# Performance work log

Hardware: AMD Instinct MI355X
Metric: run time of the kernel (lower is better)

## Reference

```python
import jax, jax.numpy as jnp
import numpy as np

N = 50000          # nodes (B-rep faces)
E = 1600000        # edges (face adjacency, avg degree 32)
GRID = 8           # UV sample grid
HEADS = 4
DH = 32            # per-head dim (heads*DH = 128)
NUM_CLASSES = 25


def _conv(x, w, b):
    # x: [N,C,H,W], w: [O,I,3,3], SAME padding, stride 1
    y = jax.lax.conv_general_dilated(x, w, (1, 1), 'SAME',
                                     dimension_numbers=('NCHW', 'OIHW', 'NCHW'))
    return y + b[None, :, None, None]


def gated_gat(x, edge_index, edge_attr, W, b, We, be, a_src, a_dst, a_edge, Wg, bg):
    # Multi-head GAT with edge-feature attention term and sigmoid edge gate.
    n = x.shape[0]
    h = (x @ W + b).reshape(n, HEADS, DH)                 # [N,H,D]
    src, dst = edge_index[0], edge_index[1]
    h_src = h[src]                                        # [E,H,D] gather
    h_dst = h[dst]                                        # [E,H,D] gather
    e_feat = (edge_attr @ We + be).reshape(-1, HEADS, DH) # [E,H,D]
    logits = jax.nn.leaky_relu(
        (h_src * a_src).sum(-1) + (h_dst * a_dst).sum(-1) + (e_feat * a_edge).sum(-1),
        negative_slope=0.2)                               # [E,H]
    # segment softmax over incoming edges of each dst node
    m = jax.ops.segment_max(logits, dst, num_segments=n)  # [N,H]
    ex = jnp.exp(logits - m[dst])
    denom = jax.ops.segment_sum(ex, dst, num_segments=n)
    alpha = ex / (denom[dst] + 1e-16)                     # [E,H]
    gate = jax.nn.sigmoid(edge_attr @ Wg + bg)            # [E,1] scalar edge gate
    msg = (h_src + e_feat) * alpha[..., None] * gate[:, :, None]  # [E,H,D]
    out = jax.ops.segment_sum(msg, dst, num_segments=n)   # [N,H,D] scatter-add
    return jax.nn.elu(out.reshape(n, HEADS * DH))


def setup_inputs() -> dict:
    key = jax.random.key(0)
    ks = jax.random.split(key, 32)
    def nrm(k, shape, s=0.05):
        return jax.random.normal(k, shape, jnp.float32) * s
    z = lambda *s: jnp.zeros(s, jnp.float32)
    return dict(
        x_vis=jax.random.normal(ks[0], (N, 6, GRID, GRID), jnp.float32),
        x_sym=jax.random.normal(ks[1], (N, 3), jnp.float32),
        edge_index=jax.random.randint(ks[2], (2, E), 0, N),
        edge_attr=jax.random.uniform(ks[3], (E, 2), jnp.float32),
        # UVEncoder: conv(6->32) -> conv(32->64) -> global avg pool -> fc(64->128)
        conv1_w=nrm(ks[4], (32, 6, 3, 3)), conv1_b=z(32),
        conv2_w=nrm(ks[5], (64, 32, 3, 3)), conv2_b=z(64),
        uvfc_w=nrm(ks[6], (64, 128)), uvfc_b=z(128),
        # SymbolicEncoder: fc(3->64) -> relu -> fc(64->64) -> relu
        sym1_w=nrm(ks[7], (3, 64)), sym1_b=z(64),
        sym2_w=nrm(ks[8], (64, 64)), sym2_b=z(64),
        # GatedGAT layer 1 (192 -> 128, heads=4, edge_dim=2)
        g1_W=nrm(ks[9], (192, 128)), g1_b=z(128),
        g1_We=nrm(ks[10], (2, 128)), g1_be=z(128),
        g1_asrc=nrm(ks[11], (HEADS, DH)), g1_adst=nrm(ks[12], (HEADS, DH)),
        g1_aedge=nrm(ks[13], (HEADS, DH)),
        g1_Wg=nrm(ks[14], (2, 1)), g1_bg=z(1),
        # GatedGAT layer 2 (128 -> 128)
        g2_W=nrm(ks[15], (128, 128)), g2_b=z(128),
        g2_We=nrm(ks[16], (2, 128)), g2_be=z(128),
        g2_asrc=nrm(ks[17], (HEADS, DH)), g2_adst=nrm(ks[18], (HEADS, DH)),
        g2_aedge=nrm(ks[19], (HEADS, DH)),
        g2_Wg=nrm(ks[20], (2, 1)), g2_bg=z(1),
        # classifier: fc(128->64) -> relu -> (dropout eval noop) -> fc(64->25)
        cls1_w=nrm(ks[21], (128, 64)), cls1_b=z(64),
        cls2_w=nrm(ks[22], (64, NUM_CLASSES)), cls2_b=z(NUM_CLASSES),
    )


def reference(x_vis, x_sym, edge_index, edge_attr,
              conv1_w, conv1_b, conv2_w, conv2_b, uvfc_w, uvfc_b,
              sym1_w, sym1_b, sym2_w, sym2_b,
              g1_W, g1_b, g1_We, g1_be, g1_asrc, g1_adst, g1_aedge, g1_Wg, g1_bg,
              g2_W, g2_b, g2_We, g2_be, g2_asrc, g2_adst, g2_aedge, g2_Wg, g2_bg,
              cls1_w, cls1_b, cls2_w, cls2_b):
    # UVEncoder
    h = jax.nn.relu(_conv(x_vis, conv1_w, conv1_b))
    h = jax.nn.relu(_conv(h, conv2_w, conv2_b))
    v_vis = h.mean(axis=(2, 3)) @ uvfc_w + uvfc_b          # [N,128]
    # SymbolicEncoder
    v_sym = jax.nn.relu(x_sym @ sym1_w + sym1_b)
    v_sym = jax.nn.relu(v_sym @ sym2_w + sym2_b)           # [N,64]
    x = jnp.concatenate([v_vis, v_sym], axis=1)            # [N,192]
    x = gated_gat(x, edge_index, edge_attr, g1_W, g1_b, g1_We, g1_be,
                  g1_asrc, g1_adst, g1_aedge, g1_Wg, g1_bg)
    x = gated_gat(x, edge_index, edge_attr, g2_W, g2_b, g2_We, g2_be,
                  g2_asrc, g2_adst, g2_aedge, g2_Wg, g2_bg)
    h = jax.nn.relu(x @ cls1_w + cls1_b)
    return h @ cls2_w + cls2_b                             # [N,25]
```

## Files before the change

kernel.cpp:

```cpp
#include <hip/hip_runtime.h>

#define NND 50000
#define NE  1600000
#define CAP 72

typedef __attribute__((ext_vector_type(8))) short bf16x8;
typedef __attribute__((ext_vector_type(4))) float f32x4;

__device__ __forceinline__ float leaky02(float x){ return x > 0.f ? x : 0.2f*x; }
__device__ __forceinline__ unsigned short f2bf(float f){
  unsigned u = __float_as_uint(f);
  u = (u + 0x7fffu + ((u >> 16) & 1u)) >> 16;
  return (unsigned short)u;
}
__device__ __forceinline__ float bf2f(unsigned short h){
  return __uint_as_float(((unsigned)h) << 16);
}
__device__ __forceinline__ unsigned cvt_pk_bf16(float lo, float hi){
  unsigned r;
  asm("v_cvt_pk_bf16_f32 %0, %1, %2" : "=v"(r) : "v"(lo), "v"(hi));
  return r;
}
__device__ __forceinline__ bf16x8 ld_frag(const unsigned short* p){
  return __builtin_bit_cast(bf16x8, *(const uint4*)p);
}

__global__ __launch_bounds__(256) void prep_mega(
    const float* __restrict__ w1, const float* __restrict__ w2,
    unsigned short* __restrict__ W1t, unsigned short* __restrict__ W2t,
    const float* __restrict__ fcw, const float* __restrict__ fcb,
    const float* __restrict__ g1W, const float* __restrict__ g1b,
    float* __restrict__ Weff, float* __restrict__ beff,
    const float* __restrict__ g2W,
    unsigned short* __restrict__ G1h, unsigned short* __restrict__ G1l,
    unsigned short* __restrict__ G2h, unsigned short* __restrict__ G2l,
    int* __restrict__ cnt)
{
  int b = blockIdx.x, t = threadIdx.x;
  if (b == 0){
    for (int i = t; i < 3072; i += 256){
      int j = i & 7, oc = (i >> 3) & 31, g = (i >> 8) & 3, m = i >> 10;
      int tap = m*4 + g;
      float v = (tap < 9 && j < 6) ? w1[oc*54 + j*9 + tap] : 0.f;
      W1t[i] = f2bf(v);
    }
  } else if (b == 1){
    for (int i = t; i < 18432; i += 256){
      int j = i & 7, oc = (i >> 3) & 63, g = (i >> 9) & 3, tap = i >> 11;
      int ic = g*8 + j;
      W2t[i] = f2bf(w2[oc*288 + ic*9 + tap]);
    }
  } else if (b < 66){
    int idx = (b - 2)*256 + t;
    int r = idx >> 7, c = idx & 127;
    float acc;
    if (r < 64){
      acc = 0.f;
      #pragma unroll 4
      for (int m = 0; m < 128; m++) acc += fcw[r*128 + m] * g1W[m*128 + c];
    } else {
      acc = g1W[(64 + r)*128 + c];
    }
    Weff[idx] = acc;
    if (b == 2 && t < 128){
      float bacc = g1b[t];
      #pragma unroll 4
      for (int m = 0; m < 128; m++) bacc = fmaf(fcb[m], g1W[m*128 + t], bacc);
      beff[t] = bacc;
    }
  } else if (b < 194){
    int sub = b - 66;
    const float* W = (sub < 64) ? Weff : g2W;
    unsigned short* Wh = (sub < 64) ? G1h : G2h;
    unsigned short* Wl = (sub < 64) ? G1l : G2l;
    int i = (sub & 63)*256 + t;
    int j = i & 7, lx = (i >> 3) & 63, nt = (i >> 9) & 7, ks = i >> 12;
    int k = ks*32 + (lx >> 4)*8 + j;
    int col = nt*16 + (lx & 15);
    float v = W[k*128 + col];
    unsigned short h16 = f2bf(v);
    Wh[i] = h16;
    Wl[i] = f2bf(v - bf2f(h16));
  } else {
    int i = (b - 194)*256 + t;
    if (i < NND) cnt[i] = 0;
  }
}

__global__ __launch_bounds__(256) void scatter_kernel(const int* __restrict__ ei,
                                                      const float* __restrict__ ea,
                                                      int* __restrict__ cnt,
                                                      int2* __restrict__ srcattr){
  int e = blockIdx.x*256 + threadIdx.x;
  if (e < NE){
    int dstn = ei[NE + e];
    int pos  = atomicAdd(&cnt[dstn], 1);
    if (pos < CAP){
      float2 a = *(const float2*)(ea + 2*e);
      unsigned pa = (unsigned)f2bf(a.x) | ((unsigned)f2bf(a.y) << 16);
      srcattr[(unsigned)dstn*CAP + pos] = make_int2(ei[e], (int)pa);
    }
  }
}

__global__ __launch_bounds__(256, 2) void uv_mfma_kernel(
    const float* __restrict__ x_vis, const float* __restrict__ x_sym,
    const unsigned short* __restrict__ W1t, const unsigned short* __restrict__ W2t,
    const float* __restrict__ b1, const float* __restrict__ b2,
    const float* __restrict__ s1w, const float* __restrict__ s1b,
    const float* __restrict__ s2w, const float* __restrict__ s2b,
    float* __restrict__ x128)
{
  __shared__ __align__(16) unsigned short xic[4*800];
  __shared__ __align__(16) unsigned short c1p[4*4000];
  __shared__ float symh[4][64];

  const int t = threadIdx.x;
  const int w = t >> 6, l = t & 63;
  const int g = l >> 4, r16 = l & 15;
  const int xb = r16 & 7, yb = r16 >> 3;
  const int n = blockIdx.x*4 + w;

  uint4 z4 = {0,0,0,0};
  if (l < 36){
    int y, x;
    if (l < 10){ y = 0; x = l; }
    else if (l < 20){ y = 9; x = l - 10; }
    else if (l < 28){ y = l - 19; x = 0; }
    else { y = l - 27; x = 9; }
    *(uint4*)(xic + w*800 + (y*10 + x)*8) = z4;
    uint4* cp = (uint4*)(c1p + w*4000 + (y*10 + x)*40);
    cp[0] = z4; cp[1] = z4; cp[2] = z4; cp[3] = z4;
  }

  {
    const float* xv = x_vis + (size_t)n*384;
    int y = l >> 3, x = l & 7;
    float v0 = xv[l], v1 = xv[64+l], v2 = xv[128+l];
    float v3 = xv[192+l], v4 = xv[256+l], v5 = xv[320+l];
    uint4 pk;
    pk.x = cvt_pk_bf16(v0, v1);
    pk.y = cvt_pk_bf16(v2, v3);
    pk.z = cvt_pk_bf16(v4, v5);
    pk.w = 0u;
    *(uint4*)(xic + w*800 + ((y+1)*10 + (x+1))*8) = pk;
  }
  asm volatile("" ::: "memory");

  uint4 B1[3][2];
  #pragma unroll
  for (int m = 0; m < 3; m++)
    #pragma unroll
    for (int nt = 0; nt < 2; nt++)
      B1[m][nt] = *(const uint4*)(W1t + m*1024 + g*256 + (nt*16 + r16)*8);

  const int t0 = g;     const int dy0 = t0/3, dx0 = t0%3;
  const int t1 = 4 + g; const int dy1 = t1/3, dx1 = t1%3;
  const int dy2 = 2, dx2 = 2;

  const float b1a = b1[r16], b1c = b1[16 + r16];
  f32x4 acc1[4][2];
  #pragma unroll
  for (int mt = 0; mt < 4; mt++){
    acc1[mt][0] = (f32x4){b1a, b1a, b1a, b1a};
    acc1[mt][1] = (f32x4){b1c, b1c, b1c, b1c};
  }
  const unsigned short* xn = xic + w*800;
  #pragma unroll
  for (int mt = 0; mt < 4; mt++){
    const int Y = mt*2 + yb;
    bf16x8 A0 = ld_frag(xn + (Y+dy0)*80 + (xb+dx0)*8);
    bf16x8 A1 = ld_frag(xn + (Y+dy1)*80 + (xb+dx1)*8);
    bf16x8 A2 = ld_frag(xn + (Y+dy2)*80 + (xb+dx2)*8);
    #pragma unroll
    for (int nt = 0; nt < 2; nt++){
      acc1[mt][nt] = __builtin_amdgcn_mfma_f32_16x16x32_bf16(A0, __builtin_bit_cast(bf16x8, B1[0][nt]), acc1[mt][nt], 0,0,0);
      acc1[mt][nt] = __builtin_amdgcn_mfma_f32_16x16x32_bf16(A1, __builtin_bit_cast(bf16x8, B1[1][nt]), acc1[mt][nt], 0,0,0);
      acc1[mt][nt] = __builtin_amdgcn_mfma_f32_16x16x32_bf16(A2, __builtin_bit_cast(bf16x8, B1[2][nt]), acc1[mt][nt], 0,0,0);
    }
  }
  unsigned short* cn = c1p + w*4000;
  #pragma unroll
  for (int mt = 0; mt < 4; mt++)
    #pragma unroll
    for (int nt = 0; nt < 2; nt++)
      #pragma unroll
      for (int jp = 0; jp < 2; jp++){
        float v0 = acc1[mt][nt][2*jp];     v0 = v0 > 0.f ? v0 : 0.f;
        float v1 = acc1[mt][nt][2*jp + 1]; v1 = v1 > 0.f ? v1 : 0.f;
        unsigned pk = cvt_pk_bf16(v0, v1);
        int r0 = g*4 + 2*jp, r1 = r0 + 1;
        int y0 = mt*2 + (r0 >> 3), x0 = r0 & 7;
        int y1 = mt*2 + (r1 >> 3), x1 = r1 & 7;
        cn[((y0+1)*10 + (x0+1))*40 + nt*16 + r16] = (unsigned short)pk;
        cn[((y1+1)*10 + (x1+1))*40 + nt*16 + r16] = (unsigned short)(pk >> 16);
      }
  asm volatile("" ::: "memory");

  float pooled4[4];
  #pragma unroll
  for (int ph = 0; ph < 2; ph++){
    const int ntA = 2*ph, ntB = 2*ph + 1;
    const float bA = b2[ntA*16 + r16], bB = b2[ntB*16 + r16];
    f32x4 accA[4], accB[4];
    #pragma unroll
    for (int mt = 0; mt < 4; mt++){
      accA[mt] = (f32x4){bA, bA, bA, bA};
      accB[mt] = (f32x4){bB, bB, bB, bB};
    }
    #pragma unroll
    for (int tap = 0; tap < 9; tap++){
      const int dy = tap/3, dx = tap%3;
      uint4 BvA = *(const uint4*)(W2t + tap*2048 + g*512 + (ntA*16 + r16)*8);
      uint4 BvB = *(const uint4*)(W2t + tap*2048 + g*512 + (ntB*16 + r16)*8);
      uint4 Av[4];
      #pragma unroll
      for (int mt = 0; mt < 4; mt++){
        int Y = mt*2 + yb + dy, X = xb + dx;
        Av[mt] = *(const uint4*)(cn + (Y*10 + X)*40 + g*8);
      }
      #pragma unroll
      for (int mt = 0; mt < 4; mt++){
        accA[mt] = __builtin_amdgcn_mfma_f32_16x16x32_bf16(
            __builtin_bit_cast(bf16x8, Av[mt]), __builtin_bit_cast(bf16x8, BvA), accA[mt], 0,0,0);
        accB[mt] = __builtin_amdgcn_mfma_f32_16x16x32_bf16(
            __builtin_bit_cast(bf16x8, Av[mt]), __builtin_bit_cast(bf16x8, BvB), accB[mt], 0,0,0);
      }
    }
    float sA = 0.f, sB = 0.f;
    #pragma unroll
    for (int mt = 0; mt < 4; mt++)
      #pragma unroll
      for (int j = 0; j < 4; j++){
        float vA = accA[mt][j]; sA += (vA > 0.f ? vA : 0.f);
        float vB = accB[mt][j]; sB += (vB > 0.f ? vB : 0.f);
      }
    pooled4[ph*2]     = sA;
    pooled4[ph*2 + 1] = sB;
  }

  float* xo = x128 + (size_t)n*128;
  #pragma unroll
  for (int k = 0; k < 4; k++){
    pooled4[k] += __shfl_xor(pooled4[k], 16);
    pooled4[k] += __shfl_xor(pooled4[k], 32);
  }
  if (l < 16){
    #pragma unroll
    for (int k = 0; k < 4; k++)
      xo[k*16 + l] = pooled4[k] * (1.f/64.f);
  }
  {
    const float* xs = x_sym + (size_t)n*3;
    float a = s1b[l] + xs[0]*s1w[l] + xs[1]*s1w[64+l] + xs[2]*s1w[128+l];
    symh[w][l] = a > 0.f ? a : 0.f;
  }
  asm volatile("" ::: "memory");
  {
    float a = s2b[l];
    #pragma unroll 8
    for (int k = 0; k < 64; k++) a = fmaf(symh[w][k], s2w[k*64 + l], a);
    xo[64 + l] = a > 0.f ? a : 0.f;
  }
}

template<int K>
__global__ __launch_bounds__(256) void node_gemm(
    const float* __restrict__ xin,
    const unsigned short* __restrict__ Wh, const unsigned short* __restrict__ Wl,
    const float* __restrict__ b,
    const float* __restrict__ asrc, const float* __restrict__ adst,
    unsigned short* __restrict__ h_out, float* __restrict__ s_out, float* __restrict__ d_out)
{
  const int w = threadIdx.x >> 6, l = threadIdx.x & 63;
  const int g = l >> 4, r16 = l & 15;
  const int rowbase = blockIdx.x*16;
  const int nt0 = 2*w, nt1 = 2*w + 1;

  f32x4 acc0, acc1;
  {
    float b0 = b[nt0*16 + r16], b1v = b[nt1*16 + r16];
    acc0 = (f32x4){b0, b0, b0, b0};
    acc1 = (f32x4){b1v, b1v, b1v, b1v};
  }

  const float* xr = xin + (size_t)(rowbase + r16)*K + g*8;
  #pragma unroll
  for (int ks = 0; ks < K/32; ks++){
    float4 xa = *(const float4*)(xr + ks*32);
    float4 xb = *(const float4*)(xr + ks*32 + 4);
    float xs[8] = {xa.x,xa.y,xa.z,xa.w,xb.x,xb.y,xb.z,xb.w};
    uint4 hpk, lpk;
    unsigned* hp = (unsigned*)&hpk;
    unsigned* lp = (unsigned*)&lpk;
    #pragma unroll
    for (int p = 0; p < 4; p++){
      unsigned ph = cvt_pk_bf16(xs[2*p], xs[2*p+1]);
      float r0 = xs[2*p]   - __uint_as_float(ph << 16);
      float r1 = xs[2*p+1] - __uint_as_float(ph & 0xffff0000u);
      hp[p] = ph;
      lp[p] = cvt_pk_bf16(r0, r1);
    }
    bf16x8 Ah = __builtin_bit_cast(bf16x8, hpk);
    bf16x8 Al = __builtin_bit_cast(bf16x8, lpk);
    const int fo0 = (((ks*8 + nt0)*64 + l)*8);
    const int fo1 = (((ks*8 + nt1)*64 + l)*8);
    bf16x8 Bh0 = ld_frag(Wh + fo0), Bl0 = ld_frag(Wl + fo0);
    bf16x8 Bh1 = ld_frag(Wh + fo1), Bl1 = ld_frag(Wl + fo1);
    acc0 = __builtin_amdgcn_mfma_f32_16x16x32_bf16(Ah, Bh0, acc0, 0,0,0);
    acc0 = __builtin_amdgcn_mfma_f32_16x16x32_bf16(Al, Bh0, acc0, 0,0,0);
    acc0 = __builtin_amdgcn_mfma_f32_16x16x32_bf16(Ah, Bl0, acc0, 0,0,0);
    acc1 = __builtin_amdgcn_mfma_f32_16x16x32_bf16(Ah, Bh1, acc1, 0,0,0);
    acc1 = __builtin_amdgcn_mfma_f32_16x16x32_bf16(Al, Bh1, acc1, 0,0,0);
    acc1 = __builtin_amdgcn_mfma_f32_16x16x32_bf16(Ah, Bl1, acc1, 0,0,0);
  }

  #pragma unroll
  for (int jp = 0; jp < 2; jp++){
    unsigned p0 = cvt_pk_bf16(acc0[2*jp], acc0[2*jp+1]);
    unsigned p1 = cvt_pk_bf16(acc1[2*jp], acc1[2*jp+1]);
    size_t ra = (size_t)(rowbase + g*4 + 2*jp)*128;
    size_t rb = (size_t)(rowbase + g*4 + 2*jp + 1)*128;
    h_out[ra + nt0*16 + r16] = (unsigned short)p0;
    h_out[rb + nt0*16 + r16] = (unsigned short)(p0 >> 16);
    h_out[ra + nt1*16 + r16] = (unsigned short)p1;
    h_out[rb + nt1*16 + r16] = (unsigned short)(p1 >> 16);
  }

  float as0 = asrc[nt0*16 + r16], as1 = asrc[nt1*16 + r16];
  float ad0 = adst[nt0*16 + r16], ad1 = adst[nt1*16 + r16];
  float sp[4], dp[4];
  #pragma unroll
  for (int j = 0; j < 4; j++){
    sp[j] = acc0[j]*as0 + acc1[j]*as1;
    dp[j] = acc0[j]*ad0 + acc1[j]*ad1;
  }
  #pragma unroll
  for (int o = 1; o < 16; o <<= 1)
    #pragma unroll
    for (int j = 0; j < 4; j++){
      sp[j] += __shfl_xor(sp[j], o);
      dp[j] += __shfl_xor(dp[j], o);
    }
  if (r16 == 0)
    #pragma unroll
    for (int j = 0; j < 4; j++)
      s_out[(rowbase + g*4 + j)*4 + w] = sp[j];
  if (r16 == 1)
    #pragma unroll
    for (int j = 0; j < 4; j++)
      d_out[(rowbase + g*4 + j)*4 + w] = dp[j];
}

template<bool FUSE_CLS>
__global__ __launch_bounds__(256) void gat_aggregate(
    const float* __restrict__ sarr, const float* __restrict__ darr,
    const unsigned short* __restrict__ hb,
    const int2* __restrict__ srcattr, const int* __restrict__ cnt,
    const float* __restrict__ We, const float* __restrict__ be,
    const float* __restrict__ aedge, const float* __restrict__ Wg, const float* __restrict__ bgp,
    float* __restrict__ xout,
    const float* __restrict__ cw1, const float* __restrict__ cb1,
    const float* __restrict__ cw2, const float* __restrict__ cb2,
    float* __restrict__ out)
{
  __shared__ int2 ew[4][2][4][64];
  __shared__ float xrow[4][128];
  __shared__ float hrow[4][64];
  const int l   = threadIdx.x & 63;
  const int w   = threadIdx.x >> 6;
  const int v   = blockIdx.x*4 + w;
  const int hd  = l >> 4;
  const int e16 = l & 15;
  const int c0  = 2*l;
  const int c8  = e16 * 8;
  const int hd2 = e16 >> 2;

  float ae0 = aedge[hd*32 + (c0 & 31)];
  float ae1 = aedge[hd*32 + ((c0+1) & 31)];
  float p0 = We[c0]*ae0 + We[c0+1]*ae1;
  float p1 = We[128+c0]*ae0 + We[128+c0+1]*ae1;
  float pc = be[c0]*ae0 + be[c0+1]*ae1;
  #pragma unroll
  for (int o = 1; o < 16; o <<= 1){ p0 += __shfl_xor(p0,o); p1 += __shfl_xor(p1,o); pc += __shfl_xor(pc,o); }
  const float wg0 = Wg[0], wg1 = Wg[1], bgv = bgp[0];

  const unsigned off = (unsigned)v * CAP;
  int deg = cnt[v]; if (deg > CAP) deg = CAP;
  const float dh = darr[(size_t)v*4 + hd];

  float dn = 0.f, Sm = 0.f, S0 = 0.f, S1 = 0.f;
  float acc[8] = {0.f,0.f,0.f,0.f,0.f,0.f,0.f,0.f};

  int pb = 0;
  for (int base = 0; base < deg; base += 64, pb ^= 1){
    #pragma unroll
    for (int s = 0; s < 4; s++){
      if (base + s*16 < deg){
        int ii = base + s*16 + e16;
        float wv = 0.f; int sj = 0;
        if (ii < deg){
          int2 sa = srcattr[off + (unsigned)ii];
          sj = sa.x;
          unsigned pa = (unsigned)sa.y;
          float a0 = __uint_as_float(pa << 16);
          float a1 = __uint_as_float(pa & 0xffff0000u);
          float sv = sarr[(unsigned)(sj*4 + hd)];
          float e  = __expf(leaky02(sv + dh + a0*p0 + a1*p1 + pc));
          float gt = 1.f/(1.f + __expf(-(a0*wg0 + a1*wg1 + bgv)));
          dn += e; wv = gt*e;
          Sm += wv; S0 += wv*a0; S1 += wv*a1;
        }
        ew[w][pb][hd][s*16 + e16] = make_int2(__float_as_int(wv), sj);
      }
    }
    asm volatile("s_waitcnt lgkmcnt(0)" ::: "memory");
    const int2* eb = &ew[w][pb][hd2][0];
    int lim = deg - base; if (lim > 64) lim = 64;
    const char* hbp = (const char*)hb;
    #pragma unroll 4
    for (int j = 0; j < lim; j += 4){
      int2 ws2 = eb[j + hd];
      float wv = __int_as_float(ws2.x);
      unsigned boff = ((unsigned)ws2.y << 8) + (unsigned)(c8 * 2);
      uint4 hv = *(const uint4*)(hbp + boff);
      acc[0] = fmaf(__uint_as_float(hv.x << 16),         wv, acc[0]);
      acc[1] = fmaf(__uint_as_float(hv.x & 0xffff0000u), wv, acc[1]);
      acc[2] = fmaf(__uint_as_float(hv.y << 16),         wv, acc[2]);
      acc[3] = fmaf(__uint_as_float(hv.y & 0xffff0000u), wv, acc[3]);
      acc[4] = fmaf(__uint_as_float(hv.z << 16),         wv, acc[4]);
      acc[5] = fmaf(__uint_as_float(hv.z & 0xffff0000u), wv, acc[5]);
      acc[6] = fmaf(__uint_as_float(hv.w << 16),         wv, acc[6]);
      acc[7] = fmaf(__uint_as_float(hv.w & 0xffff0000u), wv, acc[7]);
    }
  }

  #pragma unroll
  for (int k = 0; k < 8; k++){
    acc[k] += __shfl_xor(acc[k], 16);
    acc[k] += __shfl_xor(acc[k], 32);
  }
  #pragma unroll
  for (int o = 1; o < 16; o <<= 1){
    dn += __shfl_xor(dn, o); Sm += __shfl_xor(Sm, o);
    S0 += __shfl_xor(S0, o); S1 += __shfl_xor(S1, o);
  }
  int srcl = hd2*16 + e16;
  float den = __shfl(dn, srcl);
  float Smh = __shfl(Sm, srcl);
  float S0h = __shfl(S0, srcl);
  float S1h = __shfl(S1, srcl);
  float rden = 1.f/(den + 1e-16f);

  float o8[8];
  #pragma unroll
  for (int k = 0; k < 8; k++){
    float x = (acc[k] + be[c8+k]*Smh + We[c8+k]*S0h + We[128+c8+k]*S1h) * rden;
    o8[k] = x > 0.f ? x : (__expf(x) - 1.f);
  }

  if constexpr (!FUSE_CLS){
    if (l < 16){
      float4 lo = make_float4(o8[0], o8[1], o8[2], o8[3]);
      float4 hi = make_float4(o8[4], o8[5], o8[6], o8[7]);
      *(float4*)(xout + (size_t)v*128 + c8)     = lo;
      *(float4*)(xout + (size_t)v*128 + c8 + 4) = hi;
    }
  } else {
    if (l < 16){
      *(float4*)&xrow[w][c8]     = make_float4(o8[0], o8[1], o8[2], o8[3]);
      *(float4*)&xrow[w][c8 + 4] = make_float4(o8[4], o8[5], o8[6], o8[7]);
    }
    asm volatile("s_waitcnt lgkmcnt(0)" ::: "memory");
    float a = cb1[l];
    #pragma unroll 8
    for (int k = 0; k < 128; k++) a = fmaf(xrow[w][k], cw1[k*64 + l], a);
    hrow[w][l] = a > 0.f ? a : 0.f;
    asm volatile("s_waitcnt lgkmcnt(0)" ::: "memory");
    if (l < 25){
      float o = cb2[l];
      #pragma unroll 8
      for (int k = 0; k < 64; k++) o = fmaf(hrow[w][k], cw2[k*25 + l], o);
      out[(size_t)v*25 + l] = o;
    }
  }
}

extern "C" void kernel_launch(void* const* d_in, const int* in_sizes, int n_in,
                              void* d_out, int out_size, void* d_ws, size_t ws_size,
                              hipStream_t stream)
{
  (void)in_sizes; (void)n_in; (void)out_size; (void)ws_size;
  const float* x_vis   = (const float*)d_in[0];
  const float* x_sym   = (const float*)d_in[1];
  const int*   ei      = (const int*)  d_in[2];
  const float* ea      = (const float*)d_in[3];
  const float* c1w     = (const float*)d_in[4];
  const float* c1b     = (const float*)d_in[5];
  const float* c2w     = (const float*)d_in[6];
  const float* c2b     = (const float*)d_in[7];
  const float* fcw     = (const float*)d_in[8];
  const float* fcb     = (const float*)d_in[9];
  const float* s1w     = (const float*)d_in[10];
  const float* s1b     = (const float*)d_in[11];
  const float* s2w     = (const float*)d_in[12];
  const float* s2b     = (const float*)d_in[13];
  const float* g1W     = (const float*)d_in[14];
  const float* g1b     = (const float*)d_in[15];
  const float* g1We    = (const float*)d_in[16];
  const float* g1be    = (const float*)d_in[17];
  const float* g1asrc  = (const float*)d_in[18];
  const float* g1adst  = (const float*)d_in[19];
  const float* g1aedge = (const float*)d_in[20];
  const float* g1Wg    = (const float*)d_in[21];
  const float* g1bg    = (const float*)d_in[22];
  const float* g2W     = (const float*)d_in[23];
  const float* g2b     = (const float*)d_in[24];
  const float* g2We    = (const float*)d_in[25];
  const float* g2be    = (const float*)d_in[26];
  const float* g2asrc  = (const float*)d_in[27];
  const float* g2adst  = (const float*)d_in[28];
  const float* g2aedge = (const float*)d_in[29];
  const float* g2Wg    = (const float*)d_in[30];
  const float* g2bg    = (const float*)d_in[31];
  const float* cw1     = (const float*)d_in[32];
  const float* cb1     = (const float*)d_in[33];
  const float* cw2     = (const float*)d_in[34];
  const float* cb2     = (const float*)d_in[35];

  size_t off = 0;
  auto take = [&](size_t bytes) -> void* {
    off = (off + 255) & ~(size_t)255;
    void* p = (char*)d_ws + off;
    off += bytes;
    return p;
  };
  int*   cnt     = (int*)  take((size_t)NND*4);
  int2*  srcattr = (int2*) take((size_t)NND*CAP*8);
  float* x128    = (float*)take((size_t)NND*128*4);
  unsigned short* hb = (unsigned short*)take((size_t)NND*128*2);
  float* sbuf    = (float*)take((size_t)NND*4*4);
  float* dbuf    = (float*)take((size_t)NND*4*4);
  float* x2      = (float*)take((size_t)NND*128*4);
  unsigned short* W1t = (unsigned short*)take(3072*2);
  unsigned short* W2t = (unsigned short*)take(18432*2);
  float* Weff    = (float*)take(16384*4);
  float* beff    = (float*)take(128*4);
  unsigned short* G1h = (unsigned short*)take(16384*2);
  unsigned short* G1l = (unsigned short*)take(16384*2);
  unsigned short* G2h = (unsigned short*)take(16384*2);
  unsigned short* G2l = (unsigned short*)take(16384*2);

  prep_mega<<<66, 256, 0, stream>>>(c1w, c2w, W1t, W2t, fcw, fcb, g1W, g1b, Weff, beff,
                                    g2W, G1h, G1l, G2h, G2l, cnt);
  prep_mega<<<390, 256, 0, stream>>>(c1w, c2w, W1t, W2t, fcw, fcb, g1W, g1b, Weff, beff,
                                     g2W, G1h, G1l, G2h, G2l, cnt);

  scatter_kernel<<<(NE+255)/256, 256, 0, stream>>>(ei, ea, cnt, srcattr);

  uv_mfma_kernel<<<NND/4, 256, 0, stream>>>(x_vis, x_sym, W1t, W2t, c1b, c2b,
                                            s1w, s1b, s2w, s2b, x128);
  node_gemm<128><<<NND/16, 256, 0, stream>>>(x128, G1h, G1l, beff, g1asrc, g1adst,
                                             hb, sbuf, dbuf);
  gat_aggregate<false><<<NND/4, 256, 0, stream>>>(sbuf, dbuf, hb, srcattr, cnt,
                                                  g1We, g1be, g1aedge, g1Wg, g1bg, x2,
                                                  nullptr, nullptr, nullptr, nullptr, nullptr);
  node_gemm<128><<<NND/16, 256, 0, stream>>>(x2, G2h, G2l, g2b, g2asrc, g2adst,
                                             hb, sbuf, dbuf);
  gat_aggregate<true><<<NND/4, 256, 0, stream>>>(sbuf, dbuf, hb, srcattr, cnt,
                                                 g2We, g2be, g2aedge, g2Wg, g2bg, nullptr,
                                                 cw1, cb1, cw2, cb2, (float*)d_out);
}
```

Baseline: 524.7 us.

## Fuse edge scatter and weight splitting into UV encoder kernel launch

New measurement: 438.2 us. -16.5%, faster.

```diff
diff --git a/kernel.cpp b/kernel.cpp
--- a/kernel.cpp
+++ b/kernel.cpp
@@ -25,15 +25,12 @@
   return __builtin_bit_cast(bf16x8, *(const uint4*)p);
 }
 
-__global__ __launch_bounds__(256) void prep_mega(
+__global__ __launch_bounds__(256) void prep_a(
     const float* __restrict__ w1, const float* __restrict__ w2,
     unsigned short* __restrict__ W1t, unsigned short* __restrict__ W2t,
     const float* __restrict__ fcw, const float* __restrict__ fcb,
     const float* __restrict__ g1W, const float* __restrict__ g1b,
     float* __restrict__ Weff, float* __restrict__ beff,
-    const float* __restrict__ g2W,
-    unsigned short* __restrict__ G1h, unsigned short* __restrict__ G1l,
-    unsigned short* __restrict__ G2h, unsigned short* __restrict__ G2l,
     int* __restrict__ cnt)
 {
   int b = blockIdx.x, t = threadIdx.x;
@@ -68,8 +65,34 @@
       for (int m = 0; m < 128; m++) bacc = fmaf(fcb[m], g1W[m*128 + t], bacc);
       beff[t] = bacc;
     }
-  } else if (b < 194){
-    int sub = b - 66;
+  } else {
+    int i = (b - 66)*256 + t;
+    if (i < NND) cnt[i] = 0;
+  }
+}
+
+__global__ __launch_bounds__(256, 2) void uv_scatter_kernel(
+    const float* __restrict__ x_vis, const float* __restrict__ x_sym,
+    const unsigned short* __restrict__ W1t, const unsigned short* __restrict__ W2t,
+    const float* __restrict__ b1, const float* __restrict__ b2,
+    const float* __restrict__ s1w, const float* __restrict__ s1b,
+    const float* __restrict__ s2w, const float* __restrict__ s2b,
+    float* __restrict__ x128,
+    const int* __restrict__ ei, const float* __restrict__ ea,
+    int* __restrict__ cnt, int2* __restrict__ srcattr,
+    const float* __restrict__ Weff, const float* __restrict__ g2W,
+    unsigned short* __restrict__ G1h, unsigned short* __restrict__ G1l,
+    unsigned short* __restrict__ G2h, unsigned short* __restrict__ G2l)
+{
+  __shared__ __align__(16) unsigned short xic[4*800];
+  __shared__ __align__(16) unsigned short c1p[4*4000];
+  __shared__ float symh[4][64];
+
+  const int bx = blockIdx.x;
+  const int t  = threadIdx.x;
+
+  if (bx >= 18750){
+    int sub = bx - 18750;
     const float* W = (sub < 64) ? Weff : g2W;
     unsigned short* Wh = (sub < 64) ? G1h : G2h;
     unsigned short* Wl = (sub < 64) ? G1l : G2l;
@@ -81,45 +104,27 @@
     unsigned short h16 = f2bf(v);
     Wh[i] = h16;
     Wl[i] = f2bf(v - bf2f(h16));
-  } else {
-    int i = (b - 194)*256 + t;
-    if (i < NND) cnt[i] = 0;
-  }
-}
-
-__global__ __launch_bounds__(256) void scatter_kernel(const int* __restrict__ ei,
-                                                      const float* __restrict__ ea,
-                                                      int* __restrict__ cnt,
-                                                      int2* __restrict__ srcattr){
-  int e = blockIdx.x*256 + threadIdx.x;
-  if (e < NE){
-    int dstn = ei[NE + e];
-    int pos  = atomicAdd(&cnt[dstn], 1);
-    if (pos < CAP){
-      float2 a = *(const float2*)(ea + 2*e);
-      unsigned pa = (unsigned)f2bf(a.x) | ((unsigned)f2bf(a.y) << 16);
-      srcattr[(unsigned)dstn*CAP + pos] = make_int2(ei[e], (int)pa);
-    }
-  }
-}
-
-__global__ __launch_bounds__(256, 2) void uv_mfma_kernel(
-    const float* __restrict__ x_vis, const float* __restrict__ x_sym,
-    const unsigned short* __restrict__ W1t, const unsigned short* __restrict__ W2t,
-    const float* __restrict__ b1, const float* __restrict__ b2,
-    const float* __restrict__ s1w, const float* __restrict__ s1b,
-    const float* __restrict__ s2w, const float* __restrict__ s2b,
-    float* __restrict__ x128)
-{
-  __shared__ __align__(16) unsigned short xic[4*800];
-  __shared__ __align__(16) unsigned short c1p[4*4000];
-  __shared__ float symh[4][64];
-
-  const int t = threadIdx.x;
+    return;
+  }
+  if (bx % 3 == 0){
+    int e = (bx/3)*256 + t;
+    if (e < NE){
+      int dstn = ei[NE + e];
+      int pos  = atomicAdd(&cnt[dstn], 1);
+      if (pos < CAP){
+        float2 a = *(const float2*)(ea + 2*e);
+        unsigned pa = (unsigned)f2bf(a.x) | ((unsigned)f2bf(a.y) << 16);
+        srcattr[(unsigned)dstn*CAP + pos] = make_int2(ei[e], (int)pa);
+      }
+    }
+    return;
+  }
+
+  const int nb = (bx/3)*2 + (bx%3) - 1;
   const int w = t >> 6, l = t & 63;
   const int g = l >> 4, r16 = l & 15;
   const int xb = r16 & 7, yb = r16 >> 3;
-  const int n = blockIdx.x*4 + w;
+  const int n = nb*4 + w;
 
   uint4 z4 = {0,0,0,0};
   if (l < 36){
@@ -551,15 +556,13 @@
   unsigned short* G2h = (unsigned short*)take(16384*2);
   unsigned short* G2l = (unsigned short*)take(16384*2);
 
-  prep_mega<<<66, 256, 0, stream>>>(c1w, c2w, W1t, W2t, fcw, fcb, g1W, g1b, Weff, beff,
-                                    g2W, G1h, G1l, G2h, G2l, cnt);
-  prep_mega<<<390, 256, 0, stream>>>(c1w, c2w, W1t, W2t, fcw, fcb, g1W, g1b, Weff, beff,
-                                     g2W, G1h, G1l, G2h, G2l, cnt);
-
-  scatter_kernel<<<(NE+255)/256, 256, 0, stream>>>(ei, ea, cnt, srcattr);
-
-  uv_mfma_kernel<<<NND/4, 256, 0, stream>>>(x_vis, x_sym, W1t, W2t, c1b, c2b,
-                                            s1w, s1b, s2w, s2b, x128);
+  prep_a<<<262, 256, 0, stream>>>(c1w, c2w, W1t, W2t, fcw, fcb, g1W, g1b, Weff, beff, cnt);
+
+  uv_scatter_kernel<<<18878, 256, 0, stream>>>(x_vis, x_sym, W1t, W2t, c1b, c2b,
+                                               s1w, s1b, s2w, s2b, x128,
+                                               ei, ea, cnt, srcattr,
+                                               Weff, g2W, G1h, G1l, G2h, G2l);
+
   node_gemm<128><<<NND/16, 256, 0, stream>>>(x128, G1h, G1l, beff, g1asrc, g1adst,
                                              hb, sbuf, dbuf);
   gat_aggregate<false><<<NND/4, 256, 0, stream>>>(sbuf, dbuf, hb, srcattr, cnt,
```
